# Kernel optimization log

Hardware: AMD Instinct MI355X
Metric: run time of the kernel (lower is better)

## Reference

```python
import jax, jax.numpy as jnp
import numpy as np

N_SRC = 50000
N_DST = 50000
N_EDGES = 1_600_000
D_IN = 128
D_OUT = 128
NUM_HEADS = 8
SCALE = float((D_OUT // NUM_HEADS) ** 0.5)


def setup_inputs() -> dict:
    key = jax.random.key(0)
    ks = jax.random.split(key, 10)
    s = 1.0 / np.sqrt(D_IN)
    return {
        "src_feat": jax.random.normal(ks[0], (N_SRC, D_IN), dtype=jnp.float32),
        "dst_feat": jax.random.normal(ks[1], (N_DST, D_OUT), dtype=jnp.float32),
        "src_idx": jax.random.randint(ks[2], (N_EDGES,), 0, N_SRC, dtype=jnp.int64),
        "dst_idx": jax.random.randint(ks[3], (N_EDGES,), 0, N_DST, dtype=jnp.int64),
        "Wq": jax.random.normal(ks[4], (D_OUT, D_OUT), dtype=jnp.float32) * s,
        "bq": jnp.zeros((D_OUT,), dtype=jnp.float32),
        "Wk": jax.random.normal(ks[5], (D_OUT, D_IN), dtype=jnp.float32) * s,
        "bk": jnp.zeros((D_OUT,), dtype=jnp.float32),
        "Wv": jax.random.normal(ks[6], (D_OUT, D_IN), dtype=jnp.float32) * s,
        "bv": jnp.zeros((D_OUT,), dtype=jnp.float32),
    }


def reference(src_feat, dst_feat, src_idx, dst_idx, Wq, bq, Wk, bk, Wv, bv):
    # Node-level projections (torch Linear: x @ W.T + b)
    Q = dst_feat @ Wq.T + bq            # [N_dst, D_OUT]
    K = src_feat @ Wk.T + bk            # [N_src, D_OUT]
    V = src_feat @ Wv.T + bv            # [N_src, D_OUT]

    # Edge-wise full-dim dot-product score (heads only affect the scale)
    score = jnp.sum(Q[dst_idx] * K[src_idx], axis=-1) / SCALE  # [E]

    # Segment softmax over incoming edges of each destination node
    m = jax.ops.segment_max(score, dst_idx, num_segments=N_DST)   # [N_dst]
    e = jnp.exp(score - m[dst_idx])                               # [E]
    denom = jax.ops.segment_sum(e, dst_idx, num_segments=N_DST)   # [N_dst]
    attn = e / denom[dst_idx]                                     # [E]

    # Weighted V scatter-sum to destination nodes
    out = jax.ops.segment_sum(attn[:, None] * V[src_idx], dst_idx,
                              num_segments=N_DST)                 # [N_dst, D_OUT]
    return out
```

## Files before the change

### kernel.cpp

```cpp
#include <hip/hip_runtime.h>
#include <hip/hip_bf16.h>


#define D 128
#define E1 4096
#define BCAP 10240
#define LOG2E 1.44269504088896340736f

typedef __attribute__((ext_vector_type(8))) short bf16x8;
typedef __attribute__((ext_vector_type(4))) float f32x4;
typedef __attribute__((ext_vector_type(4))) int v4i;
typedef __attribute__((ext_vector_type(4))) unsigned v4u;

static __device__ __forceinline__ unsigned short f2bf(float f) {
  unsigned u = __float_as_uint(f);
  u += 0x7fff + ((u >> 16) & 1);
  return (unsigned short)(u >> 16);
}
static __device__ __forceinline__ float bfl(unsigned u) {
  return __uint_as_float(u << 16);
}
static __device__ __forceinline__ float bfh(unsigned u) {
  return __uint_as_float(u & 0xffff0000u);
}

template <int CTRL>
static __device__ __forceinline__ float dpp_add(float x) {
  int y = __builtin_amdgcn_update_dpp(0, __float_as_int(x), CTRL, 0xF, 0xF, false);
  return x + __int_as_float(y);
}

static __device__ __forceinline__ float dot8(const float4& qa, const float4& qb,
                                             const v4u k0, const v4u k1) {
  return (qa.x * bfl(k0.x) + qa.y * bfh(k0.x) + qa.z * bfl(k0.y) +
          qa.w * bfh(k0.y)) +
         (qb.x * bfl(k1.x) + qb.y * bfh(k1.x) + qb.z * bfl(k1.y) +
          qb.w * bfh(k1.y));
}


static __device__ __forceinline__ void cvt_w_body(
    int bx, const float* __restrict__ Wq, const float* __restrict__ Wk,
    const float* __restrict__ Wv, unsigned short* __restrict__ oq,
    unsigned short* __restrict__ ok, unsigned short* __restrict__ ov, int n) {
  int i = bx * 256 + threadIdx.x;
  if (i < n) {
    oq[i] = f2bf(Wq[i]);
    ok[i] = f2bf(Wk[i]);
    ov[i] = f2bf(Wv[i]);
  }
}

static __device__ void bin1_body(
    int bx, int* h, int* basebuf, int* cur, const int* __restrict__ src_idx,
    const int* __restrict__ dst_idx, int* __restrict__ bins,
    int* __restrict__ bcount, int n) {
  const int tid = threadIdx.x;
  const int e0 = bx * E1;
  int dv[16], sv[16];
#pragma unroll
  for (int i = 0; i < 4; ++i) {
    int e = e0 + i * 1024 + tid * 4;
    if (e + 3 < n) {
      v4i d4 = __builtin_nontemporal_load((const v4i*)(dst_idx + e));
      v4i s4 = __builtin_nontemporal_load((const v4i*)(src_idx + e));
      dv[4 * i + 0] = d4.x; dv[4 * i + 1] = d4.y;
      dv[4 * i + 2] = d4.z; dv[4 * i + 3] = d4.w;
      sv[4 * i + 0] = s4.x; sv[4 * i + 1] = s4.y;
      sv[4 * i + 2] = s4.z; sv[4 * i + 3] = s4.w;
    } else {
      for (int k = 0; k < 4; ++k) {
        int ee = e + k;
        dv[4 * i + k] = (ee < n) ? dst_idx[ee] : -1;
        sv[4 * i + k] = (ee < n) ? src_idx[ee] : 0;
      }
    }
  }
  h[tid] = 0;
  __syncthreads();
#pragma unroll
  for (int i = 0; i < 16; ++i)
    if (dv[i] >= 0) atomicAdd(&h[dv[i] >> 8], 1);
  __syncthreads();
  const int c = h[tid];
  if (c > 0) basebuf[tid] = tid * BCAP + atomicAdd(&bcount[tid], c);
  cur[tid] = 0;
  __syncthreads();
#pragma unroll
  for (int i = 0; i < 16; ++i) {
    if (dv[i] >= 0) {
      const int b = dv[i] >> 8;
      const int r = atomicAdd(&cur[b], 1);
      const int off = basebuf[b] + r;
      if (off < (b + 1) * BCAP)
        bins[off] = sv[i] | ((dv[i] & 255) << 17);
    }
  }
}

static __device__ void bin2_body(
    int b, int* smem, const int* __restrict__ bins,
    const int* __restrict__ bcount, int* __restrict__ csr,
    int* __restrict__ rowptr, int n_dst, int n_edges) {
  int* h = smem;
  int* ofs = smem + 256;
  int* cur = smem + 512;
  int* red = smem + 768;
  const int tid = threadIdx.x;
  red[tid] = (tid < b) ? min(bcount[tid], BCAP) : 0;
  __syncthreads();
  for (int off = 128; off > 0; off >>= 1) {
    if (tid < off) red[tid] += red[tid + off];
    __syncthreads();
  }
  const int gbase = red[0];
  const int cnt = min(bcount[b], BCAP);
  h[tid] = 0;
  __syncthreads();
  const int* bb = bins + b * BCAP;
  for (int i = tid; i < cnt; i += 256) atomicAdd(&h[(bb[i] >> 17) & 255], 1);
  __syncthreads();
  const int myh = h[tid];
  red[tid] = myh;
  __syncthreads();
  for (int off = 1; off < 256; off <<= 1) {
    int t = (tid >= off) ? red[tid - off] : 0;
    __syncthreads();
    red[tid] += t;
    __syncthreads();
  }
  ofs[tid] = red[tid] - myh;
  cur[tid] = 0;
  const int d = b * 256 + tid;
  if (d < n_dst) rowptr[d] = gbase + ofs[tid];
  if (b == 0 && tid == 0) rowptr[n_dst] = n_edges;
  __syncthreads();
  for (int i = tid; i < cnt; i += 256) {
    const int p = bb[i];
    const int j = (p >> 17) & 255;
    const int r = atomicAdd(&cur[j], 1);
    csr[gbase + ofs[j] + r] = p & 0x1ffff;
  }
}

static __device__ void gemm_q_body(
    int bx, const float* __restrict__ X, const unsigned short* __restrict__ Wb,
    const float* __restrict__ bias, float* __restrict__ out, int N) {
  const int lane = threadIdx.x & 63;
  const int l15 = lane & 15, quad = lane >> 4;
  const int row0 = bx * 64 + (threadIdx.x >> 6) * 16;

  f32x4 acc[8];
#pragma unroll
  for (int t = 0; t < 8; ++t) acc[t] = (f32x4){0.f, 0.f, 0.f, 0.f};

  int ar = row0 + l15;
  if (ar >= N) ar = N - 1;
  const float* ap = X + (size_t)ar * D + quad * 8;

#pragma unroll
  for (int kc = 0; kc < 4; ++kc) {
    float4 a0 = *(const float4*)(ap + kc * 32);
    float4 a1 = *(const float4*)(ap + kc * 32 + 4);
    bf16x8 a;
    a[0] = f2bf(a0.x); a[1] = f2bf(a0.y); a[2] = f2bf(a0.z); a[3] = f2bf(a0.w);
    a[4] = f2bf(a1.x); a[5] = f2bf(a1.y); a[6] = f2bf(a1.z); a[7] = f2bf(a1.w);
#pragma unroll
    for (int t = 0; t < 8; ++t) {
      bf16x8 b =
          *(const bf16x8*)(Wb + (size_t)(t * 16 + l15) * D + kc * 32 + quad * 8);
      acc[t] = __builtin_amdgcn_mfma_f32_16x16x32_bf16(a, b, acc[t], 0, 0, 0);
    }
  }
#pragma unroll
  for (int t = 0; t < 8; ++t) {
    const int c = t * 16 + l15;
    const float bc = bias[c];
#pragma unroll
    for (int r = 0; r < 4; ++r) {
      const int row = row0 + quad * 4 + r;
      if (row < N) out[(size_t)row * D + c] = acc[t][r] + bc;
    }
  }
}

static __device__ void gemm_kv_body(
    int bx, unsigned short (*stage)[256], const float* __restrict__ X,
    const unsigned short* __restrict__ Wk, const float* __restrict__ bk,
    const unsigned short* __restrict__ Wv, const float* __restrict__ bv,
    unsigned short* __restrict__ KV, int N) {
  const int tid = threadIdx.x;
  const int lane = tid & 63;
  const int l15 = lane & 15, quad = lane >> 4;
  const int wave = tid >> 6;
  const int row0 = bx * 64 + wave * 16;

  f32x4 accK[8], accV[8];
#pragma unroll
  for (int t = 0; t < 8; ++t) {
    accK[t] = (f32x4){0.f, 0.f, 0.f, 0.f};
    accV[t] = (f32x4){0.f, 0.f, 0.f, 0.f};
  }

  int ar = row0 + l15;
  if (ar >= N) ar = N - 1;
  const float* ap = X + (size_t)ar * D + quad * 8;

#pragma unroll
  for (int kc = 0; kc < 4; ++kc) {
    float4 a0 = *(const float4*)(ap + kc * 32);
    float4 a1 = *(const float4*)(ap + kc * 32 + 4);
    bf16x8 a;
    a[0] = f2bf(a0.x); a[1] = f2bf(a0.y); a[2] = f2bf(a0.z); a[3] = f2bf(a0.w);
    a[4] = f2bf(a1.x); a[5] = f2bf(a1.y); a[6] = f2bf(a1.z); a[7] = f2bf(a1.w);
#pragma unroll
    for (int t = 0; t < 8; ++t) {
      const size_t boff = (size_t)(t * 16 + l15) * D + kc * 32 + quad * 8;
      bf16x8 b0 = *(const bf16x8*)(Wk + boff);
      bf16x8 b1 = *(const bf16x8*)(Wv + boff);
      accK[t] = __builtin_amdgcn_mfma_f32_16x16x32_bf16(a, b0, accK[t], 0, 0, 0);
      accV[t] = __builtin_amdgcn_mfma_f32_16x16x32_bf16(a, b1, accV[t], 0, 0, 0);
    }
  }
#pragma unroll
  for (int t = 0; t < 8; ++t) {
    const int c = t * 16 + l15;
    const float bkc = bk[c], bvc = bv[c];
    const int ki = ((c >> 2) << 3) + (c & 3);
#pragma unroll
    for (int r = 0; r < 4; ++r) {
      const int lr = wave * 16 + quad * 4 + r;
      stage[lr][ki] = f2bf(accK[t][r] + bkc);
      stage[lr][ki + 4] = f2bf(accV[t][r] + bvc);
    }
  }
  __syncthreads();
  const int row_base = bx * 64;
#pragma unroll
  for (int i = 0; i < 8; ++i) {
    int idx = i * 256 + tid;
    int lr = idx >> 5;
    int c8 = (idx & 31) << 3;
    int grow = row_base + lr;
    if (grow < N)
      *(f32x4*)(KV + (size_t)grow * 256 + c8) = *(const f32x4*)&stage[lr][c8];
  }
}


__global__ __launch_bounds__(256) void front_kernel(
    const float* __restrict__ Wq, const float* __restrict__ Wk,
    const float* __restrict__ Wv, unsigned short* __restrict__ oq,
    unsigned short* __restrict__ ok, unsigned short* __restrict__ ov, int nw,
    const int* __restrict__ src_idx, const int* __restrict__ dst_idx,
    int* __restrict__ bins, int* __restrict__ bcount, int n_edges, int gcvt) {
  __shared__ int sh[768];
  const int b = blockIdx.x;
  if (b < gcvt) {
    cvt_w_body(b, Wq, Wk, Wv, oq, ok, ov, nw);
  } else {
    bin1_body(b - gcvt, sh, sh + 256, sh + 512, src_idx, dst_idx, bins, bcount,
              n_edges);
  }
}

__global__ __launch_bounds__(256) void mid_kernel(
    const float* __restrict__ dst_feat, const unsigned short* __restrict__ Wqb,
    const float* __restrict__ bq, float* __restrict__ Q, int n_dst,
    const float* __restrict__ src_feat, const unsigned short* __restrict__ Wkb,
    const float* __restrict__ bk, const unsigned short* __restrict__ Wvb,
    const float* __restrict__ bv, unsigned short* __restrict__ KV, int n_src,
    const int* __restrict__ bins, const int* __restrict__ bcount,
    int* __restrict__ csr, int* __restrict__ rowptr, int n_edges, int nbk,
    int gq) {
  __shared__ unsigned short stage[64][256];
  const int b = blockIdx.x;
  if (b < nbk) {
    bin2_body(b, (int*)stage, bins, bcount, csr, rowptr, n_dst, n_edges);
  } else if (b < nbk + gq) {
    gemm_q_body(b - nbk, dst_feat, Wqb, bq, Q, n_dst);
  } else {
    gemm_kv_body(b - nbk - gq, stage, src_feat, Wkb, bk, Wvb, bv, KV, n_src);
  }
}

__global__ __launch_bounds__(256) void fused_agg_kernel(
    const float* __restrict__ Q, const unsigned short* __restrict__ KV,
    const int* __restrict__ csr, const int* __restrict__ rowptr,
    float* __restrict__ out, int n_dst) {
  const int lane = threadIdx.x & 63;
  const int g = lane >> 4;
  const int gl = lane & 15;
  const int stride = gridDim.x * 4;
  const float qs = 0.25f * LOG2E;

  for (int dd = blockIdx.x * 4 + (threadIdx.x >> 6); dd < n_dst; dd += stride) {
    const int d = __builtin_amdgcn_readfirstlane(dd);
    const int start = __builtin_amdgcn_readfirstlane(rowptr[d]);
    const int n = __builtin_amdgcn_readfirstlane(rowptr[d + 1]) - start;

    float4 q0 = *(const float4*)(Q + (size_t)d * D + 4 * gl);
    float4 q1 = *(const float4*)(Q + (size_t)d * D + 64 + 4 * gl);
    q0.x *= qs; q0.y *= qs; q0.z *= qs; q0.w *= qs;
    q1.x *= qs; q1.y *= qs; q1.z *= qs; q1.w *= qs;

    f32x4 acc0 = (f32x4){0.f, 0.f, 0.f, 0.f};
    f32x4 acc1 = (f32x4){0.f, 0.f, 0.f, 0.f};
    float den = 0.f;
    const int* cp = csr + start;

    for (int base = 0; base < n; base += 64) {
      const int il = base + lane;
      const int iv = __builtin_nontemporal_load(cp + ((il < n) ? il : (n - 1)));
      const int m = min(64, n - base);
      for (int j = 0; j < m; j += 16) {
        const int s0 = __shfl(iv, j + g, 64);
        const int s1 = __shfl(iv, j + 4 + g, 64);
        const int s2 = __shfl(iv, j + 8 + g, 64);
        const int s3 = __shfl(iv, j + 12 + g, 64);
        const unsigned short* r0 = KV + (size_t)s0 * 256 + gl * 8;
        const unsigned short* r1 = KV + (size_t)s1 * 256 + gl * 8;
        const unsigned short* r2 = KV + (size_t)s2 * 256 + gl * 8;
        const unsigned short* r3 = KV + (size_t)s3 * 256 + gl * 8;
        const v4u a0 = *(const v4u*)(r0);
        const v4u a1 = *(const v4u*)(r0 + 128);
        const v4u b0 = *(const v4u*)(r1);
        const v4u b1 = *(const v4u*)(r1 + 128);
        const v4u c0 = *(const v4u*)(r2);
        const v4u c1 = *(const v4u*)(r2 + 128);
        const v4u e0 = *(const v4u*)(r3);
        const v4u e1 = *(const v4u*)(r3 + 128);

        float p0 = dot8(q0, q1, a0, a1);
        float p1 = dot8(q0, q1, b0, b1);
        float p2 = dot8(q0, q1, c0, c1);
        float p3 = dot8(q0, q1, e0, e1);

        p0 = dpp_add<0xB1>(p0);  p1 = dpp_add<0xB1>(p1);
        p2 = dpp_add<0xB1>(p2);  p3 = dpp_add<0xB1>(p3);
        p0 = dpp_add<0x4E>(p0);  p1 = dpp_add<0x4E>(p1);
        p2 = dpp_add<0x4E>(p2);  p3 = dpp_add<0x4E>(p3);
        p0 = dpp_add<0x141>(p0); p1 = dpp_add<0x141>(p1);
        p2 = dpp_add<0x141>(p2); p3 = dpp_add<0x141>(p3);
        p0 = dpp_add<0x140>(p0); p1 = dpp_add<0x140>(p1);
        p2 = dpp_add<0x140>(p2); p3 = dpp_add<0x140>(p3);

        const float w0 = (j + g < m)      ? exp2f(p0) : 0.f;
        const float w1 = (j + 4 + g < m)  ? exp2f(p1) : 0.f;
        const float w2 = (j + 8 + g < m)  ? exp2f(p2) : 0.f;
        const float w3 = (j + 12 + g < m) ? exp2f(p3) : 0.f;

        acc0[0] += w0 * bfl(a0.z) + w1 * bfl(b0.z) + w2 * bfl(c0.z) + w3 * bfl(e0.z);
        acc0[1] += w0 * bfh(a0.z) + w1 * bfh(b0.z) + w2 * bfh(c0.z) + w3 * bfh(e0.z);
        acc0[2] += w0 * bfl(a0.w) + w1 * bfl(b0.w) + w2 * bfl(c0.w) + w3 * bfl(e0.w);
        acc0[3] += w0 * bfh(a0.w) + w1 * bfh(b0.w) + w2 * bfh(c0.w) + w3 * bfh(e0.w);
        acc1[0] += w0 * bfl(a1.z) + w1 * bfl(b1.z) + w2 * bfl(c1.z) + w3 * bfl(e1.z);
        acc1[1] += w0 * bfh(a1.z) + w1 * bfh(b1.z) + w2 * bfh(c1.z) + w3 * bfh(e1.z);
        acc1[2] += w0 * bfl(a1.w) + w1 * bfl(b1.w) + w2 * bfl(c1.w) + w3 * bfl(e1.w);
        acc1[3] += w0 * bfh(a1.w) + w1 * bfh(b1.w) + w2 * bfh(c1.w) + w3 * bfh(e1.w);
        den += (w0 + w1) + (w2 + w3);
      }
    }

#pragma unroll
    for (int msk = 16; msk <= 32; msk <<= 1) {
      acc0[0] += __shfl_xor(acc0[0], msk, 64);
      acc0[1] += __shfl_xor(acc0[1], msk, 64);
      acc0[2] += __shfl_xor(acc0[2], msk, 64);
      acc0[3] += __shfl_xor(acc0[3], msk, 64);
      acc1[0] += __shfl_xor(acc1[0], msk, 64);
      acc1[1] += __shfl_xor(acc1[1], msk, 64);
      acc1[2] += __shfl_xor(acc1[2], msk, 64);
      acc1[3] += __shfl_xor(acc1[3], msk, 64);
      den += __shfl_xor(den, msk, 64);
    }

    if (lane < 16) {
      const float r = (n > 0) ? 1.0f / den : 0.f;
      f32x4 o0 = (f32x4){acc0[0] * r, acc0[1] * r, acc0[2] * r, acc0[3] * r};
      f32x4 o1 = (f32x4){acc1[0] * r, acc1[1] * r, acc1[2] * r, acc1[3] * r};
      __builtin_nontemporal_store(o0, (f32x4*)(out + (size_t)d * D + 4 * gl));
      __builtin_nontemporal_store(o1,
                                  (f32x4*)(out + (size_t)d * D + 64 + 4 * gl));
    }
  }
}

extern "C" void kernel_launch(void* const* d_in, const int* in_sizes, int n_in,
                              void* d_out, int out_size, void* d_ws,
                              size_t ws_size, hipStream_t stream) {
  const float* src_feat = (const float*)d_in[0];
  const float* dst_feat = (const float*)d_in[1];
  const int* src_idx = (const int*)d_in[2];
  const int* dst_idx = (const int*)d_in[3];
  const float* Wq = (const float*)d_in[4];
  const float* bq = (const float*)d_in[5];
  const float* Wk = (const float*)d_in[6];
  const float* bk = (const float*)d_in[7];
  const float* Wv = (const float*)d_in[8];
  const float* bv = (const float*)d_in[9];

  const int n_src = in_sizes[0] / D;
  const int n_dst = in_sizes[1] / D;
  const int n_edges = in_sizes[2];
  const int nbk = (n_dst + 255) >> 8;

  float* out = (float*)d_out;

  float* Q = (float*)d_ws;
  unsigned short* KV = (unsigned short*)(Q + (size_t)n_dst * D);
  unsigned short* Wqb = KV + (size_t)n_src * 256;
  unsigned short* Wkb = Wqb + D * D;
  unsigned short* Wvb = Wkb + D * D;
  int* bcount = (int*)(Wvb + D * D);
  int* rowptr = bcount + 256;
  int* csr = rowptr + (n_dst + 1);
  int* bins = csr + n_edges;

  (void)hipMemsetAsync(bcount, 0, 256 * sizeof(int), stream);

  dim3 blk(256);
  const int gcvt = (D * D + 255) / 256;
  const int g1 = (n_edges + E1 - 1) / E1;
  const int gq = (n_dst + 63) / 64;
  const int gkv = (n_src + 63) / 64;

  front_kernel<<<dim3(gcvt + g1), blk, 0, stream>>>(
      Wq, Wk, Wv, Wqb, Wkb, Wvb, D * D, src_idx, dst_idx, bins, bcount,
      n_edges, gcvt);

  mid_kernel<<<dim3(nbk + gq + gkv), blk, 0, stream>>>(
      dst_feat, Wqb, bq, Q, n_dst, src_feat, Wkb, bk, Wvb, bv, KV, n_src, bins,
      bcount, csr, rowptr, n_edges, nbk, gq);

  int gfa = (n_dst + 3) / 4;
  if (gfa > 2048) gfa = 2048;
  fused_agg_kernel<<<dim3(gfa), blk, 0, stream>>>(Q, KV, csr, rowptr, out,
                                                  n_dst);
}
```

Measured before the change: 291.0 us.

## Rebalance binning: larger bin1 chunks, split bin2 buckets, one-node-per-wave aggregation

bin1 now processes 16384 edges per block using two passes over the indices: it histograms first, then re-reads the indices and scatters them. This means fewer blocks contend on the global bcount atomics, at the cost of loading the index arrays twice. bin2 is split into two blocks per bucket, each writing only half of the destination rows, which doubles parallelism but duplicates the bucket scan and histogram work. The aggregation kernel drops its grid-stride loop and launches one wave per destination node, aiming at better load balance at the cost of more blocks.

```diff
diff --git a/kernel.cpp b/kernel.cpp
--- a/kernel.cpp
+++ b/kernel.cpp
@@ -3,7 +3,7 @@
 
 
 #define D 128
-#define E1 4096
+#define E1 16384
 #define BCAP 10240
 #define LOG2E 1.44269504088896340736f
 
@@ -57,49 +57,58 @@
     int* __restrict__ bcount, int n) {
   const int tid = threadIdx.x;
   const int e0 = bx * E1;
-  int dv[16], sv[16];
-#pragma unroll
-  for (int i = 0; i < 4; ++i) {
-    int e = e0 + i * 1024 + tid * 4;
+  h[tid] = 0;
+  __syncthreads();
+  for (int t = tid; t < E1 / 4; t += 256) {
+    const int e = e0 + t * 4;
     if (e + 3 < n) {
-      v4i d4 = __builtin_nontemporal_load((const v4i*)(dst_idx + e));
-      v4i s4 = __builtin_nontemporal_load((const v4i*)(src_idx + e));
-      dv[4 * i + 0] = d4.x; dv[4 * i + 1] = d4.y;
-      dv[4 * i + 2] = d4.z; dv[4 * i + 3] = d4.w;
-      sv[4 * i + 0] = s4.x; sv[4 * i + 1] = s4.y;
-      sv[4 * i + 2] = s4.z; sv[4 * i + 3] = s4.w;
+      v4i d4 = *(const v4i*)(dst_idx + e);
+      atomicAdd(&h[d4.x >> 8], 1);
+      atomicAdd(&h[d4.y >> 8], 1);
+      atomicAdd(&h[d4.z >> 8], 1);
+      atomicAdd(&h[d4.w >> 8], 1);
     } else {
-      for (int k = 0; k < 4; ++k) {
-        int ee = e + k;
-        dv[4 * i + k] = (ee < n) ? dst_idx[ee] : -1;
-        sv[4 * i + k] = (ee < n) ? src_idx[ee] : 0;
-      }
-    }
-  }
-  h[tid] = 0;
-  __syncthreads();
-#pragma unroll
-  for (int i = 0; i < 16; ++i)
-    if (dv[i] >= 0) atomicAdd(&h[dv[i] >> 8], 1);
+      for (int k = 0; k < 4; ++k)
+        if (e + k < n) atomicAdd(&h[dst_idx[e + k] >> 8], 1);
+    }
+  }
   __syncthreads();
   const int c = h[tid];
   if (c > 0) basebuf[tid] = tid * BCAP + atomicAdd(&bcount[tid], c);
   cur[tid] = 0;
   __syncthreads();
-#pragma unroll
-  for (int i = 0; i < 16; ++i) {
-    if (dv[i] >= 0) {
-      const int b = dv[i] >> 8;
-      const int r = atomicAdd(&cur[b], 1);
-      const int off = basebuf[b] + r;
-      if (off < (b + 1) * BCAP)
-        bins[off] = sv[i] | ((dv[i] & 255) << 17);
+  for (int t = tid; t < E1 / 4; t += 256) {
+    const int e = e0 + t * 4;
+    if (e + 3 < n) {
+      v4i d4 = *(const v4i*)(dst_idx + e);
+      v4i s4 = *(const v4i*)(src_idx + e);
+      int dd[4] = {d4.x, d4.y, d4.z, d4.w};
+      int ss[4] = {s4.x, s4.y, s4.z, s4.w};
+#pragma unroll
+      for (int k = 0; k < 4; ++k) {
+        const int b = dd[k] >> 8;
+        const int r = atomicAdd(&cur[b], 1);
+        const int off = basebuf[b] + r;
+        if (off < (b + 1) * BCAP)
+          bins[off] = ss[k] | ((dd[k] & 255) << 17);
+      }
+    } else {
+      for (int k = 0; k < 4; ++k) {
+        if (e + k < n) {
+          const int dv = dst_idx[e + k];
+          const int b = dv >> 8;
+          const int r = atomicAdd(&cur[b], 1);
+          const int off = basebuf[b] + r;
+          if (off < (b + 1) * BCAP)
+            bins[off] = src_idx[e + k] | ((dv & 255) << 17);
+        }
+      }
     }
   }
 }
 
 static __device__ void bin2_body(
-    int b, int* smem, const int* __restrict__ bins,
+    int bucket, int half, int* smem, const int* __restrict__ bins,
     const int* __restrict__ bcount, int* __restrict__ csr,
     int* __restrict__ rowptr, int n_dst, int n_edges) {
   int* h = smem;
@@ -107,17 +116,17 @@
   int* cur = smem + 512;
   int* red = smem + 768;
   const int tid = threadIdx.x;
-  red[tid] = (tid < b) ? min(bcount[tid], BCAP) : 0;
+  red[tid] = (tid < bucket) ? min(bcount[tid], BCAP) : 0;
   __syncthreads();
   for (int off = 128; off > 0; off >>= 1) {
     if (tid < off) red[tid] += red[tid + off];
     __syncthreads();
   }
   const int gbase = red[0];
-  const int cnt = min(bcount[b], BCAP);
+  const int cnt = min(bcount[bucket], BCAP);
   h[tid] = 0;
   __syncthreads();
-  const int* bb = bins + b * BCAP;
+  const int* bb = bins + bucket * BCAP;
   for (int i = tid; i < cnt; i += 256) atomicAdd(&h[(bb[i] >> 17) & 255], 1);
   __syncthreads();
   const int myh = h[tid];
@@ -131,15 +140,17 @@
   }
   ofs[tid] = red[tid] - myh;
   cur[tid] = 0;
-  const int d = b * 256 + tid;
-  if (d < n_dst) rowptr[d] = gbase + ofs[tid];
-  if (b == 0 && tid == 0) rowptr[n_dst] = n_edges;
+  const int d = bucket * 256 + tid;
+  if ((tid >> 7) == half && d < n_dst) rowptr[d] = gbase + ofs[tid];
+  if (bucket == 0 && half == 0 && tid == 0) rowptr[n_dst] = n_edges;
   __syncthreads();
   for (int i = tid; i < cnt; i += 256) {
     const int p = bb[i];
     const int j = (p >> 17) & 255;
-    const int r = atomicAdd(&cur[j], 1);
-    csr[gbase + ofs[j] + r] = p & 0x1ffff;
+    if ((j >> 7) == half) {
+      const int r = atomicAdd(&cur[j], 1);
+      csr[gbase + ofs[j] + r] = p & 0x1ffff;
+    }
   }
 }
 
@@ -275,12 +286,14 @@
     int gq) {
   __shared__ unsigned short stage[64][256];
   const int b = blockIdx.x;
-  if (b < nbk) {
-    bin2_body(b, (int*)stage, bins, bcount, csr, rowptr, n_dst, n_edges);
-  } else if (b < nbk + gq) {
-    gemm_q_body(b - nbk, dst_feat, Wqb, bq, Q, n_dst);
+  if (b < 2 * nbk) {
+    bin2_body(b >> 1, b & 1, (int*)stage, bins, bcount, csr, rowptr, n_dst,
+              n_edges);
+  } else if (b < 2 * nbk + gq) {
+    gemm_q_body(b - 2 * nbk, dst_feat, Wqb, bq, Q, n_dst);
   } else {
-    gemm_kv_body(b - nbk - gq, stage, src_feat, Wkb, bk, Wvb, bv, KV, n_src);
+    gemm_kv_body(b - 2 * nbk - gq, stage, src_feat, Wkb, bk, Wvb, bv, KV,
+                 n_src);
   }
 }
 
@@ -291,98 +304,96 @@
   const int lane = threadIdx.x & 63;
   const int g = lane >> 4;
   const int gl = lane & 15;
-  const int stride = gridDim.x * 4;
+  int d = blockIdx.x * 4 + (threadIdx.x >> 6);
+  if (d >= n_dst) return;
+  d = __builtin_amdgcn_readfirstlane(d);
+  const int start = __builtin_amdgcn_readfirstlane(rowptr[d]);
+  const int n = __builtin_amdgcn_readfirstlane(rowptr[d + 1]) - start;
+
   const float qs = 0.25f * LOG2E;
-
-  for (int dd = blockIdx.x * 4 + (threadIdx.x >> 6); dd < n_dst; dd += stride) {
-    const int d = __builtin_amdgcn_readfirstlane(dd);
-    const int start = __builtin_amdgcn_readfirstlane(rowptr[d]);
-    const int n = __builtin_amdgcn_readfirstlane(rowptr[d + 1]) - start;
-
-    float4 q0 = *(const float4*)(Q + (size_t)d * D + 4 * gl);
-    float4 q1 = *(const float4*)(Q + (size_t)d * D + 64 + 4 * gl);
-    q0.x *= qs; q0.y *= qs; q0.z *= qs; q0.w *= qs;
-    q1.x *= qs; q1.y *= qs; q1.z *= qs; q1.w *= qs;
-
-    f32x4 acc0 = (f32x4){0.f, 0.f, 0.f, 0.f};
-    f32x4 acc1 = (f32x4){0.f, 0.f, 0.f, 0.f};
-    float den = 0.f;
-    const int* cp = csr + start;
-
-    for (int base = 0; base < n; base += 64) {
-      const int il = base + lane;
-      const int iv = __builtin_nontemporal_load(cp + ((il < n) ? il : (n - 1)));
-      const int m = min(64, n - base);
-      for (int j = 0; j < m; j += 16) {
-        const int s0 = __shfl(iv, j + g, 64);
-        const int s1 = __shfl(iv, j + 4 + g, 64);
-        const int s2 = __shfl(iv, j + 8 + g, 64);
-        const int s3 = __shfl(iv, j + 12 + g, 64);
-        const unsigned short* r0 = KV + (size_t)s0 * 256 + gl * 8;
-        const unsigned short* r1 = KV + (size_t)s1 * 256 + gl * 8;
-        const unsigned short* r2 = KV + (size_t)s2 * 256 + gl * 8;
-        const unsigned short* r3 = KV + (size_t)s3 * 256 + gl * 8;
-        const v4u a0 = *(const v4u*)(r0);
-        const v4u a1 = *(const v4u*)(r0 + 128);
-        const v4u b0 = *(const v4u*)(r1);
-        const v4u b1 = *(const v4u*)(r1 + 128);
-        const v4u c0 = *(const v4u*)(r2);
-        const v4u c1 = *(const v4u*)(r2 + 128);
-        const v4u e0 = *(const v4u*)(r3);
-        const v4u e1 = *(const v4u*)(r3 + 128);
-
-        float p0 = dot8(q0, q1, a0, a1);
-        float p1 = dot8(q0, q1, b0, b1);
-        float p2 = dot8(q0, q1, c0, c1);
-        float p3 = dot8(q0, q1, e0, e1);
-
-        p0 = dpp_add<0xB1>(p0);  p1 = dpp_add<0xB1>(p1);
-        p2 = dpp_add<0xB1>(p2);  p3 = dpp_add<0xB1>(p3);
-        p0 = dpp_add<0x4E>(p0);  p1 = dpp_add<0x4E>(p1);
-        p2 = dpp_add<0x4E>(p2);  p3 = dpp_add<0x4E>(p3);
-        p0 = dpp_add<0x141>(p0); p1 = dpp_add<0x141>(p1);
-        p2 = dpp_add<0x141>(p2); p3 = dpp_add<0x141>(p3);
-        p0 = dpp_add<0x140>(p0); p1 = dpp_add<0x140>(p1);
-        p2 = dpp_add<0x140>(p2); p3 = dpp_add<0x140>(p3);
-
-        const float w0 = (j + g < m)      ? exp2f(p0) : 0.f;
-        const float w1 = (j + 4 + g < m)  ? exp2f(p1) : 0.f;
-        const float w2 = (j + 8 + g < m)  ? exp2f(p2) : 0.f;
-        const float w3 = (j + 12 + g < m) ? exp2f(p3) : 0.f;
-
-        acc0[0] += w0 * bfl(a0.z) + w1 * bfl(b0.z) + w2 * bfl(c0.z) + w3 * bfl(e0.z);
-        acc0[1] += w0 * bfh(a0.z) + w1 * bfh(b0.z) + w2 * bfh(c0.z) + w3 * bfh(e0.z);
-        acc0[2] += w0 * bfl(a0.w) + w1 * bfl(b0.w) + w2 * bfl(c0.w) + w3 * bfl(e0.w);
-        acc0[3] += w0 * bfh(a0.w) + w1 * bfh(b0.w) + w2 * bfh(c0.w) + w3 * bfh(e0.w);
-        acc1[0] += w0 * bfl(a1.z) + w1 * bfl(b1.z) + w2 * bfl(c1.z) + w3 * bfl(e1.z);
-        acc1[1] += w0 * bfh(a1.z) + w1 * bfh(b1.z) + w2 * bfh(c1.z) + w3 * bfh(e1.z);
-        acc1[2] += w0 * bfl(a1.w) + w1 * bfl(b1.w) + w2 * bfl(c1.w) + w3 * bfl(e1.w);
-        acc1[3] += w0 * bfh(a1.w) + w1 * bfh(b1.w) + w2 * bfh(c1.w) + w3 * bfh(e1.w);
-        den += (w0 + w1) + (w2 + w3);
-      }
-    }
-
-#pragma unroll
-    for (int msk = 16; msk <= 32; msk <<= 1) {
-      acc0[0] += __shfl_xor(acc0[0], msk, 64);
-      acc0[1] += __shfl_xor(acc0[1], msk, 64);
-      acc0[2] += __shfl_xor(acc0[2], msk, 64);
-      acc0[3] += __shfl_xor(acc0[3], msk, 64);
-      acc1[0] += __shfl_xor(acc1[0], msk, 64);
-      acc1[1] += __shfl_xor(acc1[1], msk, 64);
-      acc1[2] += __shfl_xor(acc1[2], msk, 64);
-      acc1[3] += __shfl_xor(acc1[3], msk, 64);
-      den += __shfl_xor(den, msk, 64);
-    }
-
-    if (lane < 16) {
-      const float r = (n > 0) ? 1.0f / den : 0.f;
-      f32x4 o0 = (f32x4){acc0[0] * r, acc0[1] * r, acc0[2] * r, acc0[3] * r};
-      f32x4 o1 = (f32x4){acc1[0] * r, acc1[1] * r, acc1[2] * r, acc1[3] * r};
-      __builtin_nontemporal_store(o0, (f32x4*)(out + (size_t)d * D + 4 * gl));
-      __builtin_nontemporal_store(o1,
-                                  (f32x4*)(out + (size_t)d * D + 64 + 4 * gl));
-    }
+  float4 q0 = *(const float4*)(Q + (size_t)d * D + 4 * gl);
+  float4 q1 = *(const float4*)(Q + (size_t)d * D + 64 + 4 * gl);
+  q0.x *= qs; q0.y *= qs; q0.z *= qs; q0.w *= qs;
+  q1.x *= qs; q1.y *= qs; q1.z *= qs; q1.w *= qs;
+
+  f32x4 acc0 = (f32x4){0.f, 0.f, 0.f, 0.f};
+  f32x4 acc1 = (f32x4){0.f, 0.f, 0.f, 0.f};
+  float den = 0.f;
+  const int* cp = csr + start;
+
+  for (int base = 0; base < n; base += 64) {
+    const int il = base + lane;
+    const int iv = __builtin_nontemporal_load(cp + ((il < n) ? il : (n - 1)));
+    const int m = min(64, n - base);
+    for (int j = 0; j < m; j += 16) {
+      const int s0 = __shfl(iv, j + g, 64);
+      const int s1 = __shfl(iv, j + 4 + g, 64);
+      const int s2 = __shfl(iv, j + 8 + g, 64);
+      const int s3 = __shfl(iv, j + 12 + g, 64);
+      const unsigned short* r0 = KV + (size_t)s0 * 256 + gl * 8;
+      const unsigned short* r1 = KV + (size_t)s1 * 256 + gl * 8;
+      const unsigned short* r2 = KV + (size_t)s2 * 256 + gl * 8;
+      const unsigned short* r3 = KV + (size_t)s3 * 256 + gl * 8;
+      const v4u a0 = *(const v4u*)(r0);
+      const v4u a1 = *(const v4u*)(r0 + 128);
+      const v4u b0 = *(const v4u*)(r1);
+      const v4u b1 = *(const v4u*)(r1 + 128);
+      const v4u c0 = *(const v4u*)(r2);
+      const v4u c1 = *(const v4u*)(r2 + 128);
+      const v4u e0 = *(const v4u*)(r3);
+      const v4u e1 = *(const v4u*)(r3 + 128);
+
+      float p0 = dot8(q0, q1, a0, a1);
+      float p1 = dot8(q0, q1, b0, b1);
+      float p2 = dot8(q0, q1, c0, c1);
+      float p3 = dot8(q0, q1, e0, e1);
+
+      p0 = dpp_add<0xB1>(p0);  p1 = dpp_add<0xB1>(p1);
+      p2 = dpp_add<0xB1>(p2);  p3 = dpp_add<0xB1>(p3);
+      p0 = dpp_add<0x4E>(p0);  p1 = dpp_add<0x4E>(p1);
+      p2 = dpp_add<0x4E>(p2);  p3 = dpp_add<0x4E>(p3);
+      p0 = dpp_add<0x141>(p0); p1 = dpp_add<0x141>(p1);
+      p2 = dpp_add<0x141>(p2); p3 = dpp_add<0x141>(p3);
+      p0 = dpp_add<0x140>(p0); p1 = dpp_add<0x140>(p1);
+      p2 = dpp_add<0x140>(p2); p3 = dpp_add<0x140>(p3);
+
+      const float w0 = (j + g < m)      ? exp2f(p0) : 0.f;
+      const float w1 = (j + 4 + g < m)  ? exp2f(p1) : 0.f;
+      const float w2 = (j + 8 + g < m)  ? exp2f(p2) : 0.f;
+      const float w3 = (j + 12 + g < m) ? exp2f(p3) : 0.f;
+
+      acc0[0] += w0 * bfl(a0.z) + w1 * bfl(b0.z) + w2 * bfl(c0.z) + w3 * bfl(e0.z);
+      acc0[1] += w0 * bfh(a0.z) + w1 * bfh(b0.z) + w2 * bfh(c0.z) + w3 * bfh(e0.z);
+      acc0[2] += w0 * bfl(a0.w) + w1 * bfl(b0.w) + w2 * bfl(c0.w) + w3 * bfl(e0.w);
+      acc0[3] += w0 * bfh(a0.w) + w1 * bfh(b0.w) + w2 * bfh(c0.w) + w3 * bfh(e0.w);
+      acc1[0] += w0 * bfl(a1.z) + w1 * bfl(b1.z) + w2 * bfl(c1.z) + w3 * bfl(e1.z);
+      acc1[1] += w0 * bfh(a1.z) + w1 * bfh(b1.z) + w2 * bfh(c1.z) + w3 * bfh(e1.z);
+      acc1[2] += w0 * bfl(a1.w) + w1 * bfl(b1.w) + w2 * bfl(c1.w) + w3 * bfl(e1.w);
+      acc1[3] += w0 * bfh(a1.w) + w1 * bfh(b1.w) + w2 * bfh(c1.w) + w3 * bfh(e1.w);
+      den += (w0 + w1) + (w2 + w3);
+    }
+  }
+
+#pragma unroll
+  for (int msk = 16; msk <= 32; msk <<= 1) {
+    acc0[0] += __shfl_xor(acc0[0], msk, 64);
+    acc0[1] += __shfl_xor(acc0[1], msk, 64);
+    acc0[2] += __shfl_xor(acc0[2], msk, 64);
+    acc0[3] += __shfl_xor(acc0[3], msk, 64);
+    acc1[0] += __shfl_xor(acc1[0], msk, 64);
+    acc1[1] += __shfl_xor(acc1[1], msk, 64);
+    acc1[2] += __shfl_xor(acc1[2], msk, 64);
+    acc1[3] += __shfl_xor(acc1[3], msk, 64);
+    den += __shfl_xor(den, msk, 64);
+  }
+
+  if (lane < 16) {
+    const float r = (n > 0) ? 1.0f / den : 0.f;
+    f32x4 o0 = (f32x4){acc0[0] * r, acc0[1] * r, acc0[2] * r, acc0[3] * r};
+    f32x4 o1 = (f32x4){acc1[0] * r, acc1[1] * r, acc1[2] * r, acc1[3] * r};
+    __builtin_nontemporal_store(o0, (f32x4*)(out + (size_t)d * D + 4 * gl));
+    __builtin_nontemporal_store(o1,
+                                (f32x4*)(out + (size_t)d * D + 64 + 4 * gl));
   }
 }
 
@@ -429,12 +440,11 @@
       Wq, Wk, Wv, Wqb, Wkb, Wvb, D * D, src_idx, dst_idx, bins, bcount,
       n_edges, gcvt);
 
-  mid_kernel<<<dim3(nbk + gq + gkv), blk, 0, stream>>>(
+  mid_kernel<<<dim3(2 * nbk + gq + gkv), blk, 0, stream>>>(
       dst_feat, Wqb, bq, Q, n_dst, src_feat, Wkb, bk, Wvb, bv, KV, n_src, bins,
       bcount, csr, rowptr, n_edges, nbk, gq);
 
-  int gfa = (n_dst + 3) / 4;
-  if (gfa > 2048) gfa = 2048;
-  fused_agg_kernel<<<dim3(gfa), blk, 0, stream>>>(Q, KV, csr, rowptr, out,
-                                                  n_dst);
-}
+  fused_agg_kernel<<<dim3((n_dst + 3) / 4), blk, 0, stream>>>(Q, KV, csr,
+                                                              rowptr, out,
+                                                              n_dst);
+}
```

Measured after the change: 298.5 us. 2.6% more time.

## Fuse all stages into one cooperative persistent kernel with grid syncs

Applied to the files above, without the earlier changes.

Replaces the memset plus three kernel launches with one cooperative persistent kernel that runs weight conversion and binning, then CSR build and projections, then aggregation, separated by grid-wide syncs. The aim is to remove launch gaps and the tails between dependent kernels. In exchange, the grid is capped by occupancy, so each phase runs as grid-stride loops over fewer blocks. It also adds host-side occupancy and device-property queries on every call and falls back to the old path if the cooperative launch fails.

```diff
diff --git a/kernel.cpp b/kernel.cpp
--- a/kernel.cpp
+++ b/kernel.cpp
@@ -1,5 +1,8 @@
 #include <hip/hip_runtime.h>
 #include <hip/hip_bf16.h>
+#include <hip/hip_cooperative_groups.h>
+
+namespace cg = cooperative_groups;
 
 
 #define D 128
@@ -245,6 +248,157 @@
     if (grow < N)
       *(f32x4*)(KV + (size_t)grow * 256 + c8) = *(const f32x4*)&stage[lr][c8];
   }
+}
+
+static __device__ void fused_body(
+    int v, const float* __restrict__ Q, const unsigned short* __restrict__ KV,
+    const int* __restrict__ csr, const int* __restrict__ rowptr,
+    float* __restrict__ out, int n_dst) {
+  const int lane = threadIdx.x & 63;
+  const int g = lane >> 4;
+  const int gl = lane & 15;
+  int d = v * 4 + (threadIdx.x >> 6);
+  if (d >= n_dst) return;
+  d = __builtin_amdgcn_readfirstlane(d);
+  const int start = __builtin_amdgcn_readfirstlane(rowptr[d]);
+  const int n = __builtin_amdgcn_readfirstlane(rowptr[d + 1]) - start;
+
+  const float qs = 0.25f * LOG2E;
+  float4 q0 = *(const float4*)(Q + (size_t)d * D + 4 * gl);
+  float4 q1 = *(const float4*)(Q + (size_t)d * D + 64 + 4 * gl);
+  q0.x *= qs; q0.y *= qs; q0.z *= qs; q0.w *= qs;
+  q1.x *= qs; q1.y *= qs; q1.z *= qs; q1.w *= qs;
+
+  f32x4 acc0 = (f32x4){0.f, 0.f, 0.f, 0.f};
+  f32x4 acc1 = (f32x4){0.f, 0.f, 0.f, 0.f};
+  float den = 0.f;
+  const int* cp = csr + start;
+
+  for (int base = 0; base < n; base += 64) {
+    const int il = base + lane;
+    const int iv = __builtin_nontemporal_load(cp + ((il < n) ? il : (n - 1)));
+    const int m = min(64, n - base);
+    for (int j = 0; j < m; j += 16) {
+      const int s0 = __shfl(iv, j + g, 64);
+      const int s1 = __shfl(iv, j + 4 + g, 64);
+      const int s2 = __shfl(iv, j + 8 + g, 64);
+      const int s3 = __shfl(iv, j + 12 + g, 64);
+      const unsigned short* r0 = KV + (size_t)s0 * 256 + gl * 8;
+      const unsigned short* r1 = KV + (size_t)s1 * 256 + gl * 8;
+      const unsigned short* r2 = KV + (size_t)s2 * 256 + gl * 8;
+      const unsigned short* r3 = KV + (size_t)s3 * 256 + gl * 8;
+      const v4u a0 = *(const v4u*)(r0);
+      const v4u a1 = *(const v4u*)(r0 + 128);
+      const v4u b0 = *(const v4u*)(r1);
+      const v4u b1 = *(const v4u*)(r1 + 128);
+      const v4u c0 = *(const v4u*)(r2);
+      const v4u c1 = *(const v4u*)(r2 + 128);
+      const v4u e0 = *(const v4u*)(r3);
+      const v4u e1 = *(const v4u*)(r3 + 128);
+
+      float p0 = dot8(q0, q1, a0, a1);
+      float p1 = dot8(q0, q1, b0, b1);
+      float p2 = dot8(q0, q1, c0, c1);
+      float p3 = dot8(q0, q1, e0, e1);
+
+      p0 = dpp_add<0xB1>(p0);  p1 = dpp_add<0xB1>(p1);
+      p2 = dpp_add<0xB1>(p2);  p3 = dpp_add<0xB1>(p3);
+      p0 = dpp_add<0x4E>(p0);  p1 = dpp_add<0x4E>(p1);
+      p2 = dpp_add<0x4E>(p2);  p3 = dpp_add<0x4E>(p3);
+      p0 = dpp_add<0x141>(p0); p1 = dpp_add<0x141>(p1);
+      p2 = dpp_add<0x141>(p2); p3 = dpp_add<0x141>(p3);
+      p0 = dpp_add<0x140>(p0); p1 = dpp_add<0x140>(p1);
+      p2 = dpp_add<0x140>(p2); p3 = dpp_add<0x140>(p3);
+
+      const float w0 = (j + g < m)      ? exp2f(p0) : 0.f;
+      const float w1 = (j + 4 + g < m)  ? exp2f(p1) : 0.f;
+      const float w2 = (j + 8 + g < m)  ? exp2f(p2) : 0.f;
+      const float w3 = (j + 12 + g < m) ? exp2f(p3) : 0.f;
+
+      acc0[0] += w0 * bfl(a0.z) + w1 * bfl(b0.z) + w2 * bfl(c0.z) + w3 * bfl(e0.z);
+      acc0[1] += w0 * bfh(a0.z) + w1 * bfh(b0.z) + w2 * bfh(c0.z) + w3 * bfh(e0.z);
+      acc0[2] += w0 * bfl(a0.w) + w1 * bfl(b0.w) + w2 * bfl(c0.w) + w3 * bfl(e0.w);
+      acc0[3] += w0 * bfh(a0.w) + w1 * bfh(b0.w) + w2 * bfh(c0.w) + w3 * bfh(e0.w);
+      acc1[0] += w0 * bfl(a1.z) + w1 * bfl(b1.z) + w2 * bfl(c1.z) + w3 * bfl(e1.z);
+      acc1[1] += w0 * bfh(a1.z) + w1 * bfh(b1.z) + w2 * bfh(c1.z) + w3 * bfh(e1.z);
+      acc1[2] += w0 * bfl(a1.w) + w1 * bfl(b1.w) + w2 * bfl(c1.w) + w3 * bfl(e1.w);
+      acc1[3] += w0 * bfh(a1.w) + w1 * bfh(b1.w) + w2 * bfh(c1.w) + w3 * bfh(e1.w);
+      den += (w0 + w1) + (w2 + w3);
+    }
+  }
+
+#pragma unroll
+  for (int msk = 16; msk <= 32; msk <<= 1) {
+    acc0[0] += __shfl_xor(acc0[0], msk, 64);
+    acc0[1] += __shfl_xor(acc0[1], msk, 64);
+    acc0[2] += __shfl_xor(acc0[2], msk, 64);
+    acc0[3] += __shfl_xor(acc0[3], msk, 64);
+    acc1[0] += __shfl_xor(acc1[0], msk, 64);
+    acc1[1] += __shfl_xor(acc1[1], msk, 64);
+    acc1[2] += __shfl_xor(acc1[2], msk, 64);
+    acc1[3] += __shfl_xor(acc1[3], msk, 64);
+    den += __shfl_xor(den, msk, 64);
+  }
+
+  if (lane < 16) {
+    const float r = (n > 0) ? 1.0f / den : 0.f;
+    f32x4 o0 = (f32x4){acc0[0] * r, acc0[1] * r, acc0[2] * r, acc0[3] * r};
+    f32x4 o1 = (f32x4){acc1[0] * r, acc1[1] * r, acc1[2] * r, acc1[3] * r};
+    __builtin_nontemporal_store(o0, (f32x4*)(out + (size_t)d * D + 4 * gl));
+    __builtin_nontemporal_store(o1,
+                                (f32x4*)(out + (size_t)d * D + 64 + 4 * gl));
+  }
+}
+
+
+struct MegaArgs {
+  const float* Wq; const float* Wk; const float* Wv;
+  unsigned short* Wqb; unsigned short* Wkb; unsigned short* Wvb;
+  const int* src_idx; const int* dst_idx;
+  int* bins; int* bcount;
+  const float* dst_feat; const float* src_feat;
+  const float* bq; const float* bk; const float* bv;
+  float* Qm; unsigned short* KV;
+  int* csr; int* rowptr;
+  float* out;
+  int n_src, n_dst, n_edges, nbk, gcvt, g1, gq, gkv, nf;
+};
+
+__global__ __launch_bounds__(256, 4) void mega_kernel(MegaArgs a) {
+  cg::grid_group grid = cg::this_grid();
+  __shared__ unsigned short stage[64][256];
+  int* sh = (int*)stage;
+
+  if (blockIdx.x == 0) a.bcount[threadIdx.x] = 0;
+  __threadfence();
+  grid.sync();
+
+  for (int v = blockIdx.x; v < a.gcvt + a.g1; v += gridDim.x) {
+    __syncthreads();
+    if (v < a.gcvt)
+      cvt_w_body(v, a.Wq, a.Wk, a.Wv, a.Wqb, a.Wkb, a.Wvb, D * D);
+    else
+      bin1_body(v - a.gcvt, sh, sh + 256, sh + 512, a.src_idx, a.dst_idx,
+                a.bins, a.bcount, a.n_edges);
+  }
+  __threadfence();
+  grid.sync();
+
+  for (int v = blockIdx.x; v < a.nbk + a.gq + a.gkv; v += gridDim.x) {
+    __syncthreads();
+    if (v < a.nbk)
+      bin2_body(v, sh, a.bins, a.bcount, a.csr, a.rowptr, a.n_dst, a.n_edges);
+    else if (v < a.nbk + a.gq)
+      gemm_q_body(v - a.nbk, a.dst_feat, a.Wqb, a.bq, a.Qm, a.n_dst);
+    else
+      gemm_kv_body(v - a.nbk - a.gq, stage, a.src_feat, a.Wkb, a.bk, a.Wvb,
+                   a.bv, a.KV, a.n_src);
+  }
+  __threadfence();
+  grid.sync();
+
+  for (int v = blockIdx.x; v < a.nf; v += gridDim.x)
+    fused_body(v, a.Qm, a.KV, a.csr, a.rowptr, a.out, a.n_dst);
 }
 
 
@@ -288,102 +442,7 @@
     const float* __restrict__ Q, const unsigned short* __restrict__ KV,
     const int* __restrict__ csr, const int* __restrict__ rowptr,
     float* __restrict__ out, int n_dst) {
-  const int lane = threadIdx.x & 63;
-  const int g = lane >> 4;
-  const int gl = lane & 15;
-  const int stride = gridDim.x * 4;
-  const float qs = 0.25f * LOG2E;
-
-  for (int dd = blockIdx.x * 4 + (threadIdx.x >> 6); dd < n_dst; dd += stride) {
-    const int d = __builtin_amdgcn_readfirstlane(dd);
-    const int start = __builtin_amdgcn_readfirstlane(rowptr[d]);
-    const int n = __builtin_amdgcn_readfirstlane(rowptr[d + 1]) - start;
-
-    float4 q0 = *(const float4*)(Q + (size_t)d * D + 4 * gl);
-    float4 q1 = *(const float4*)(Q + (size_t)d * D + 64 + 4 * gl);
-    q0.x *= qs; q0.y *= qs; q0.z *= qs; q0.w *= qs;
-    q1.x *= qs; q1.y *= qs; q1.z *= qs; q1.w *= qs;
-
-    f32x4 acc0 = (f32x4){0.f, 0.f, 0.f, 0.f};
-    f32x4 acc1 = (f32x4){0.f, 0.f, 0.f, 0.f};
-    float den = 0.f;
-    const int* cp = csr + start;
-
-    for (int base = 0; base < n; base += 64) {
-      const int il = base + lane;
-      const int iv = __builtin_nontemporal_load(cp + ((il < n) ? il : (n - 1)));
-      const int m = min(64, n - base);
-      for (int j = 0; j < m; j += 16) {
-        const int s0 = __shfl(iv, j + g, 64);
-        const int s1 = __shfl(iv, j + 4 + g, 64);
-        const int s2 = __shfl(iv, j + 8 + g, 64);
-        const int s3 = __shfl(iv, j + 12 + g, 64);
-        const unsigned short* r0 = KV + (size_t)s0 * 256 + gl * 8;
-        const unsigned short* r1 = KV + (size_t)s1 * 256 + gl * 8;
-        const unsigned short* r2 = KV + (size_t)s2 * 256 + gl * 8;
-        const unsigned short* r3 = KV + (size_t)s3 * 256 + gl * 8;
-        const v4u a0 = *(const v4u*)(r0);
-        const v4u a1 = *(const v4u*)(r0 + 128);
-        const v4u b0 = *(const v4u*)(r1);
-        const v4u b1 = *(const v4u*)(r1 + 128);
-        const v4u c0 = *(const v4u*)(r2);
-        const v4u c1 = *(const v4u*)(r2 + 128);
-        const v4u e0 = *(const v4u*)(r3);
-        const v4u e1 = *(const v4u*)(r3 + 128);
-
-        float p0 = dot8(q0, q1, a0, a1);
-        float p1 = dot8(q0, q1, b0, b1);
-        float p2 = dot8(q0, q1, c0, c1);
-        float p3 = dot8(q0, q1, e0, e1);
-
-        p0 = dpp_add<0xB1>(p0);  p1 = dpp_add<0xB1>(p1);
-        p2 = dpp_add<0xB1>(p2);  p3 = dpp_add<0xB1>(p3);
-        p0 = dpp_add<0x4E>(p0);  p1 = dpp_add<0x4E>(p1);
-        p2 = dpp_add<0x4E>(p2);  p3 = dpp_add<0x4E>(p3);
-        p0 = dpp_add<0x141>(p0); p1 = dpp_add<0x141>(p1);
-        p2 = dpp_add<0x141>(p2); p3 = dpp_add<0x141>(p3);
-        p0 = dpp_add<0x140>(p0); p1 = dpp_add<0x140>(p1);
-        p2 = dpp_add<0x140>(p2); p3 = dpp_add<0x140>(p3);
-
-        const float w0 = (j + g < m)      ? exp2f(p0) : 0.f;
-        const float w1 = (j + 4 + g < m)  ? exp2f(p1) : 0.f;
-        const float w2 = (j + 8 + g < m)  ? exp2f(p2) : 0.f;
-        const float w3 = (j + 12 + g < m) ? exp2f(p3) : 0.f;
-
-        acc0[0] += w0 * bfl(a0.z) + w1 * bfl(b0.z) + w2 * bfl(c0.z) + w3 * bfl(e0.z);
-        acc0[1] += w0 * bfh(a0.z) + w1 * bfh(b0.z) + w2 * bfh(c0.z) + w3 * bfh(e0.z);
-        acc0[2] += w0 * bfl(a0.w) + w1 * bfl(b0.w) + w2 * bfl(c0.w) + w3 * bfl(e0.w);
-        acc0[3] += w0 * bfh(a0.w) + w1 * bfh(b0.w) + w2 * bfh(c0.w) + w3 * bfh(e0.w);
-        acc1[0] += w0 * bfl(a1.z) + w1 * bfl(b1.z) + w2 * bfl(c1.z) + w3 * bfl(e1.z);
-        acc1[1] += w0 * bfh(a1.z) + w1 * bfh(b1.z) + w2 * bfh(c1.z) + w3 * bfh(e1.z);
-        acc1[2] += w0 * bfl(a1.w) + w1 * bfl(b1.w) + w2 * bfl(c1.w) + w3 * bfl(e1.w);
-        acc1[3] += w0 * bfh(a1.w) + w1 * bfh(b1.w) + w2 * bfh(c1.w) + w3 * bfh(e1.w);
-        den += (w0 + w1) + (w2 + w3);
-      }
-    }
-
-#pragma unroll
-    for (int msk = 16; msk <= 32; msk <<= 1) {
-      acc0[0] += __shfl_xor(acc0[0], msk, 64);
-      acc0[1] += __shfl_xor(acc0[1], msk, 64);
-      acc0[2] += __shfl_xor(acc0[2], msk, 64);
-      acc0[3] += __shfl_xor(acc0[3], msk, 64);
-      acc1[0] += __shfl_xor(acc1[0], msk, 64);
-      acc1[1] += __shfl_xor(acc1[1], msk, 64);
-      acc1[2] += __shfl_xor(acc1[2], msk, 64);
-      acc1[3] += __shfl_xor(acc1[3], msk, 64);
-      den += __shfl_xor(den, msk, 64);
-    }
-
-    if (lane < 16) {
-      const float r = (n > 0) ? 1.0f / den : 0.f;
-      f32x4 o0 = (f32x4){acc0[0] * r, acc0[1] * r, acc0[2] * r, acc0[3] * r};
-      f32x4 o1 = (f32x4){acc1[0] * r, acc1[1] * r, acc1[2] * r, acc1[3] * r};
-      __builtin_nontemporal_store(o0, (f32x4*)(out + (size_t)d * D + 4 * gl));
-      __builtin_nontemporal_store(o1,
-                                  (f32x4*)(out + (size_t)d * D + 64 + 4 * gl));
-    }
-  }
+  fused_body(blockIdx.x, Q, KV, csr, rowptr, out, n_dst);
 }
 
 extern "C" void kernel_launch(void* const* d_in, const int* in_sizes, int n_in,
@@ -417,24 +476,54 @@
   int* csr = rowptr + (n_dst + 1);
   int* bins = csr + n_edges;
 
-  (void)hipMemsetAsync(bcount, 0, 256 * sizeof(int), stream);
-
-  dim3 blk(256);
   const int gcvt = (D * D + 255) / 256;
   const int g1 = (n_edges + E1 - 1) / E1;
   const int gq = (n_dst + 63) / 64;
   const int gkv = (n_src + 63) / 64;
-
-  front_kernel<<<dim3(gcvt + g1), blk, 0, stream>>>(
-      Wq, Wk, Wv, Wqb, Wkb, Wvb, D * D, src_idx, dst_idx, bins, bcount,
-      n_edges, gcvt);
-
-  mid_kernel<<<dim3(nbk + gq + gkv), blk, 0, stream>>>(
-      dst_feat, Wqb, bq, Q, n_dst, src_feat, Wkb, bk, Wvb, bv, KV, n_src, bins,
-      bcount, csr, rowptr, n_edges, nbk, gq);
-
-  int gfa = (n_dst + 3) / 4;
-  if (gfa > 2048) gfa = 2048;
-  fused_agg_kernel<<<dim3(gfa), blk, 0, stream>>>(Q, KV, csr, rowptr, out,
-                                                  n_dst);
-}
+  const int nf = (n_dst + 3) / 4;
+
+  MegaArgs a;
+  a.Wq = Wq; a.Wk = Wk; a.Wv = Wv;
+  a.Wqb = Wqb; a.Wkb = Wkb; a.Wvb = Wvb;
+  a.src_idx = src_idx; a.dst_idx = dst_idx;
+  a.bins = bins; a.bcount = bcount;
+  a.dst_feat = dst_feat; a.src_feat = src_feat;
+  a.bq = bq; a.bk = bk; a.bv = bv;
+  a.Qm = Q; a.KV = KV;
+  a.csr = csr; a.rowptr = rowptr;
+  a.out = out;
+  a.n_src = n_src; a.n_dst = n_dst; a.n_edges = n_edges; a.nbk = nbk;
+  a.gcvt = gcvt; a.g1 = g1; a.gq = gq; a.gkv = gkv; a.nf = nf;
+
+  int nb = 0;
+  hipError_t qe = hipOccupancyMaxActiveBlocksPerMultiprocessor(
+      &nb, (const void*)mega_kernel, 256, 0);
+  int ncu = 256;
+  hipDeviceProp_t prop;
+  int dev = 0;
+  if (hipGetDevice(&dev) == hipSuccess &&
+      hipGetDeviceProperties(&prop, dev) == hipSuccess)
+    ncu = prop.multiProcessorCount;
+  int cgrid = (qe == hipSuccess && nb > 0) ? nb * ncu : 0;
+  if (cgrid > 4096) cgrid = 4096;
+
+  hipError_t le = hipErrorUnknown;
+  if (cgrid > 0) {
+    void* kp[] = {(void*)&a};
+    le = hipLaunchCooperativeKernel((const void*)mega_kernel, dim3(cgrid),
+                                    dim3(256), kp, 0, stream);
+  }
+
+  if (le != hipSuccess) {
+    dim3 blk(256);
+    (void)hipMemsetAsync(bcount, 0, 256 * sizeof(int), stream);
+    front_kernel<<<dim3(gcvt + g1), blk, 0, stream>>>(
+        Wq, Wk, Wv, Wqb, Wkb, Wvb, D * D, src_idx, dst_idx, bins, bcount,
+        n_edges, gcvt);
+    mid_kernel<<<dim3(nbk + gq + gkv), blk, 0, stream>>>(
+        dst_feat, Wqb, bq, Q, n_dst, src_feat, Wkb, bk, Wvb, bv, KV, n_src,
+        bins, bcount, csr, rowptr, n_edges, nbk, gq);
+    fused_agg_kernel<<<dim3(nf), blk, 0, stream>>>(Q, KV, csr, rowptr, out,
+                                                   n_dst);
+  }
+}
```

New measurement: 307.4 us. 1.06x slower.
